# Kernel tuning notes

Hardware: AMD Instinct MI355X
Metric: run time of the kernel (lower is better)

The kernel has to match this reference:

```python
import jax, jax.numpy as jnp
import numpy as np

NUM_M = 2_000_000
NUM_T = 512
N = 16
NUM_GEN = N * (N - 1) // 2  # 120
NUM_STEPS = 64
TAU = 1.0


def _make_bases():
    # skew-symmetric so(n) basis, matching the torch buffer construction order
    bases = np.zeros((NUM_GEN, N, N), np.float32)
    k = 0
    for i in range(N):
        for j in range(i + 1, N):
            bases[k, i, j] = -1.0
            bases[k, j, i] = 1.0
            k += 1
    return jnp.asarray(bases)


def setup_inputs() -> dict:
    key = jax.random.key(0)
    ks = jax.random.split(key, 8)
    W = jax.random.normal(ks[0], (NUM_M, N), jnp.float32)
    emb_weight = W / jnp.linalg.norm(W, axis=-1, keepdims=True)  # normalized at init
    transition_coeffs = jax.random.normal(ks[1], (NUM_T, NUM_GEN), jnp.float32) * 0.1

    def lin(k, fi, fo):  # torch nn.Linear default init
        bound = 1.0 / np.sqrt(fi)
        kw, kb = jax.random.split(k)
        w = jax.random.uniform(kw, (fi, fo), jnp.float32, -bound, bound)
        b = jax.random.uniform(kb, (fo,), jnp.float32, -bound, bound)
        return w, b

    w1, b1 = lin(ks[2], 2 * N, 256)
    w2, b2 = lin(ks[3], 256, 128)
    w3, b3 = lin(ks[4], 128, NUM_T)

    v_src = jax.random.uniform(ks[5], (1, NUM_M), jnp.float32)
    v_target = jax.random.uniform(ks[6], (1, NUM_M), jnp.float32)
    # pre-sampled Gumbel(0,1) noise for gumbel_softmax, one draw per step
    u = jax.random.uniform(ks[7], (NUM_STEPS, 1, NUM_T), jnp.float32, 1e-6, 1.0 - 1e-6)
    gumbel = -jnp.log(-jnp.log(u))

    return {
        'v_src': v_src, 'v_target': v_target,
        'emb_weight': emb_weight, 'transition_coeffs': transition_coeffs,
        'bases': _make_bases(),
        'w1': w1, 'b1': b1, 'w2': w2, 'b2': b2, 'w3': w3, 'b3': b3,
        'gumbel': gumbel, 'num_steps': NUM_STEPS,
    }


def reference(v_src, v_target, emb_weight, transition_coeffs, bases,
              w1, b1, w2, b2, w3, b3, gumbel, num_steps):
    # training=True path of PetriNetAlignmentPredictor.forward, tau=1.0
    embs = emb_weight / jnp.linalg.norm(emb_weight, axis=-1, keepdims=True)
    v_cur = v_src @ embs      # [1, n]  (memory-bound matvec over num_m)
    v_tgt = v_target @ embs   # [1, n]
    gens = jnp.einsum('tg,gnm->tnm', transition_coeffs, bases)  # [num_t, n, n]
    expm_b = jax.vmap(jax.scipy.linalg.expm)

    def step(v, g):
        h = jax.nn.relu(jnp.concatenate([v, v_tgt], axis=-1) @ w1 + b1)
        h = jax.nn.relu(h @ w2 + b2)
        logits = h @ w3 + b3                       # [1, num_t]
        # gumbel_softmax(hard=True) with straight-through estimator
        y = jax.nn.softmax((logits + g) / TAU, axis=-1)
        hard = jax.nn.one_hot(jnp.argmax(y, axis=-1), logits.shape[-1], dtype=y.dtype)
        one_hot = hard + y - jax.lax.stop_gradient(y)
        omega = jnp.einsum('bt,tnm->bnm', one_hot, gens)  # skew-symmetric [1, n, n]
        R = expm_b(omega)
        v2 = jnp.einsum('bnm,bm->bn', R, v)
        v2 = v2 / jnp.linalg.norm(v2, axis=-1, keepdims=True)
        return v2, logits

    v_fin, logits_seq = jax.lax.scan(step, v_cur, gumbel[:num_steps])
    pred_marking = jax.nn.softmax(v_fin @ embs.T, axis=-1)  # [1, num_m]
    return pred_marking, logits_seq[:, 0, :]  # squeeze batch dim -> [num_steps, num_t]
```

## Files before the change

### kernel.cpp

```cpp
#include <hip/hip_runtime.h>

#define M_TOTAL   2000000
#define NT        512
#define K1_BLOCKS 1024
#define K3_BLOCKS 2048

__device__ __forceinline__ float rlf(float v, int l) {
    union { float f; int i; } u; u.f = v;
    u.i = __builtin_amdgcn_readlane(u.i, l);
    return u.f;
}

__device__ __forceinline__ void bar_lds() {
    asm volatile("s_waitcnt lgkmcnt(0)" ::: "memory");
    __builtin_amdgcn_s_barrier();
    asm volatile("" ::: "memory");
}

#define DPPMAXU(m, ctrl) { unsigned _d = (unsigned)__builtin_amdgcn_update_dpp(0, (int)(m), (ctrl), 0xF, 0xF, true); \
                           if (_d > (m)) (m) = _d; }
#define DPPADDF(s, ctrl) { float _d = __int_as_float(__builtin_amdgcn_update_dpp(0, __float_as_int(s), (ctrl), 0xF, 0xF, true)); \
                           (s) += _d; }

__device__ __forceinline__ unsigned orderf(float f) {
    unsigned u = __float_as_uint(f);
    return u ^ (((unsigned)((int)u >> 31)) | 0x80000000u);
}

__device__ __forceinline__ uint2 pick2(uint2 a, uint2 b) {
    bool takeb = (b.x > a.x) || (b.x == a.x && b.y < a.y);
    return takeb ? b : a;
}

#define REP16(M)  M(0) M(1) M(2) M(3) M(4) M(5) M(6) M(7) M(8) M(9) M(10) M(11) M(12) M(13) M(14) M(15)
#define REP16B(M) M(16) M(17) M(18) M(19) M(20) M(21) M(22) M(23) M(24) M(25) M(26) M(27) M(28) M(29) M(30) M(31)

#define VLD4(dst, base, c) { const volatile float* _p = (base) + 4*(c); \
    dst.x = _p[0]; dst.y = _p[1]; dst.z = _p[2]; dst.w = _p[3]; }

extern "C" __global__ __launch_bounds__(256)
void k_reduce(const float* __restrict__ emb, const float* __restrict__ vsrc,
              const float* __restrict__ vtgt, double* __restrict__ partials)
{
    const int tid = threadIdx.x;
    const int bid = blockIdx.x;
    double aS[4], aT[4];
#pragma unroll
    for (int i = 0; i < 4; i++) { aS[i] = 0.0; aT[i] = 0.0; }

    const float4* emb4 = (const float4*)emb;
    for (long long f = (long long)bid * 256 + tid; f < (long long)M_TOTAL * 4;
         f += (long long)K1_BLOCKS * 256) {
        float4 e = emb4[f];
        long long r = f >> 2;
        float sq = fmaf(e.x, e.x, fmaf(e.y, e.y, fmaf(e.z, e.z, e.w * e.w)));
        sq += __shfl_xor(sq, 1);
        sq += __shfl_xor(sq, 2);
        float invn = 1.0f / sqrtf(sq);
        float s = vsrc[r] * invn;
        float t = vtgt[r] * invn;
        aS[0] += (double)(s * e.x); aS[1] += (double)(s * e.y);
        aS[2] += (double)(s * e.z); aS[3] += (double)(s * e.w);
        aT[0] += (double)(t * e.x); aT[1] += (double)(t * e.y);
        aT[2] += (double)(t * e.z); aT[3] += (double)(t * e.w);
    }
#pragma unroll
    for (int i = 0; i < 4; i++) {
#pragma unroll
        for (int off = 32; off >= 4; off >>= 1) {
            aS[i] += __shfl_down(aS[i], off);
            aT[i] += __shfl_down(aT[i], off);
        }
    }
    __shared__ double lred[4][32];
    int lane = tid & 63, wv = tid >> 6;
    if (lane < 4) {
#pragma unroll
        for (int i = 0; i < 4; i++) {
            lred[wv][lane * 4 + i]      = aS[i];
            lred[wv][16 + lane * 4 + i] = aT[i];
        }
    }
    __syncthreads();
    if (tid < 32) {
        double v = lred[0][tid] + lred[1][tid] + lred[2][tid] + lred[3][tid];
        partials[(long long)bid * 32 + tid] = v;
    }
}

extern "C" __global__ __launch_bounds__(256)
void k_pre(const float* __restrict__ tc, float* __restrict__ Rtab,
           const float* __restrict__ w2g, const float* __restrict__ w3g,
           float* __restrict__ w2R, float* __restrict__ w3R,
           double* __restrict__ totalp)
{
    const int bid = blockIdx.x;
    const int t = threadIdx.x;

    if (bid < 512) {
        const int i = t >> 4, j = t & 15;
        __shared__ float Om[256];
        __shared__ float Ms[256];

        const float* crow = tc + bid * 120;
        float o = 0.0f;
        if (i < j)      o = -crow[(i * (31 - i)) / 2 + (j - i - 1)];
        else if (i > j) o =  crow[(j * (31 - j)) / 2 + (i - j - 1)];
        Om[t] = o;
        Ms[t] = o;
        float s = (i == j ? 1.0f : 0.0f) + o;
        __syncthreads();

#pragma unroll
        for (int k = 2; k <= 16; k++) {
            float a0 = 0.0f, a1 = 0.0f, a2 = 0.0f, a3 = 0.0f;
#pragma unroll
            for (int m = 0; m < 4; m++) {
                a0 = fmaf(Om[i * 16 + m],      Ms[m * 16 + j],        a0);
                a1 = fmaf(Om[i * 16 + 4 + m],  Ms[(4 + m) * 16 + j],  a1);
                a2 = fmaf(Om[i * 16 + 8 + m],  Ms[(8 + m) * 16 + j],  a2);
                a3 = fmaf(Om[i * 16 + 12 + m], Ms[(12 + m) * 16 + j], a3);
            }
            float acc = ((a0 + a1) + (a2 + a3)) * (1.0f / (float)k);
            __syncthreads();
            Ms[t] = acc;
            s += acc;
            __syncthreads();
        }
        Rtab[bid * 256 + t] = s;
    } else {
        if (bid == 512 && t == 0) totalp[0] = 0.0;
        if (t >= 128) return;
        const int b = bid - 512;
        const int k = t;
        if (b < 512) {
            w3R[b * 128 + k] = w3g[k * 512 + b];
        } else {
            const int p2 = b - 512;
            const int j2 = k;
            for (int m = 0; m < 64; m++)
                w2R[(((p2 << 7) | j2) * 64) + m] = w2g[(64 * p2 + m) * 128 + j2];
        }
    }
}

extern "C" __global__ __launch_bounds__(512)
__attribute__((amdgpu_waves_per_eu(2, 2)))
void k_steps(const double* __restrict__ partials,
             const float* __restrict__ w1g, const float* __restrict__ b1g,
             const float* __restrict__ b2g, const float* __restrict__ b3g,
             const float* __restrict__ w2R, const float* __restrict__ w3R,
             const float* __restrict__ Rtab, const float* __restrict__ gum,
             const int* __restrict__ nsp,
             float* __restrict__ outL, float* __restrict__ vf_out)
{
    __shared__ __align__(16) float h1s[256];
    __shared__ __align__(16) float h2p[512];
    __shared__ __align__(16) float h2s[128];
    __shared__ float xs[32];
    __shared__ float b2s[128];
    __shared__ uint2 kidx[8];
    __shared__ double dred[512];

    const int t = threadIdx.x;
    const int lane = t & 63;
    const int wv = t >> 6;
    const int j2 = t & 127, p2 = t >> 7;
    const int c1 = t & 255;

    const volatile float* w3v = (const volatile float*)(w3R + (size_t)t * 128);
    const volatile float* w2v = (const volatile float*)(w2R + (size_t)t * 64);
#define W3D(c) float4 w3_##c; VLD4(w3_##c, w3v, c)
    REP16(W3D) REP16B(W3D)
#undef W3D
#define W2D(c) float4 w2_##c; VLD4(w2_##c, w2v, c)
    REP16(W2D)
#undef W2D
    const float b3r = b3g[t];

    float w1r[16];
    {
        const volatile float* w1v = (const volatile float*)w1g;
#pragma unroll
        for (int m = 0; m < 16; m++) w1r[m] = w1v[m * 256 + c1];
    }
    if (t < 128) b2s[t] = b2g[t];

    float warm = 0.0f;
    for (int i = t; i < 512 * 256 / 4; i += 512) {
        float4 rv = ((const float4*)Rtab)[i];
        warm += (rv.x + rv.y) + (rv.z + rv.w);
    }

    {
        double v = 0.0;
#pragma unroll 4
        for (int i = 0; i < (K1_BLOCKS * 32) / 512; i++) v += partials[i * 512 + t];
        dred[t] = v;
    }

    int ns = nsp[0];
    if (ns > 64) ns = 64;
    if (ns < 0)  ns = 0;
    if (ns == -2147483647) vf_out[0] = warm;

    __syncthreads();
    if (t < 32) {
        double s = 0.0;
#pragma unroll
        for (int j = 0; j < 16; j++) s += dred[t + 32 * j];
        xs[t] = (float)s;
    }
    __syncthreads();

    float b1e = 0.0f, vreg = 0.0f;
    if (t < 256) {
        float a = b1g[c1];
#pragma unroll
        for (int m = 0; m < 16; m++)
            a = fmaf(xs[16 + m], w1g[(16 + m) * 256 + c1], a);
        b1e = a;
        vreg = xs[lane & 15];
    }

    if (ns == 0 && t < 16) vf_out[t] = xs[t];

    for (int step = 0; step < ns; step++) {
        float gv = gum[step * 512 + t];

        if (t < 256) {
            float a0 = 0.0f, a1 = 0.0f;
#pragma unroll
            for (int m = 0; m < 8; m++) {
                a0 = fmaf(rlf(vreg, m),     w1r[m],     a0);
                a1 = fmaf(rlf(vreg, 8 + m), w1r[8 + m], a1);
            }
            h1s[t] = fmaxf((a0 + a1) + b1e, 0.0f);
        }
        bar_lds();

        {
            const float2* h1b = (const float2*)&h1s[p2 << 6];
            float a0 = 0.0f, a1 = 0.0f, a2 = 0.0f, a3 = 0.0f;
#define L2C(c) { float2 mA = h1b[2*(c)]; float2 mB = h1b[2*(c)+1]; \
                 a0 = fmaf(mA.x, w2_##c.x, a0); \
                 a1 = fmaf(mA.y, w2_##c.y, a1); \
                 a2 = fmaf(mB.x, w2_##c.z, a2); \
                 a3 = fmaf(mB.y, w2_##c.w, a3); }
            REP16(L2C)
#undef L2C
            h2p[(p2 << 7) | j2] = (a0 + a1) + (a2 + a3);
        }
        bar_lds();

        if (t < 128) {
            float s = ((h2p[t] + h2p[128 + t]) + (h2p[256 + t] + h2p[384 + t])) + b2s[t];
            h2s[t] = fmaxf(s, 0.0f);
        }
        bar_lds();

        float lg;
        {
            const float2* h2b = (const float2*)h2s;
            float lg0 = 0.0f, lg1 = 0.0f, lg2 = 0.0f, lg3 = 0.0f;
#define L3C(c) { float2 mA = h2b[2*(c)]; float2 mB = h2b[2*(c)+1]; \
                 lg0 = fmaf(mA.x, w3_##c.x, lg0); \
                 lg1 = fmaf(mA.y, w3_##c.y, lg1); \
                 lg2 = fmaf(mB.x, w3_##c.z, lg2); \
                 lg3 = fmaf(mB.y, w3_##c.w, lg3); }
            REP16(L3C) REP16B(L3C)
#undef L3C
            lg = ((lg0 + lg1) + (lg2 + lg3)) + b3r;
        }
        outL[step * 512 + t] = lg;

        {
            unsigned ok = orderf(lg + gv);
            unsigned m = ok;
            DPPMAXU(m, 0x111)
            DPPMAXU(m, 0x112)
            DPPMAXU(m, 0x114)
            DPPMAXU(m, 0x118)
            DPPMAXU(m, 0x142)
            DPPMAXU(m, 0x143)
            unsigned wmax = (unsigned)__builtin_amdgcn_readlane((int)m, 63);
            unsigned long long mask = __ballot(ok == wmax);
            if (lane == 0) {
                uint2 kv; kv.x = wmax; kv.y = (unsigned)(wv * 64 + (__ffsll(mask) - 1));
                kidx[wv] = kv;
            }
        }
        bar_lds();

        if (t < 256 && lane < 16) {
            uint2 K0, K1, K2, K3, K4, K5, K6, K7;
            { uint4 a = *(const uint4*)&kidx[0]; K0.x=a.x; K0.y=a.y; K1.x=a.z; K1.y=a.w; }
            { uint4 a = *(const uint4*)&kidx[2]; K2.x=a.x; K2.y=a.y; K3.x=a.z; K3.y=a.w; }
            { uint4 a = *(const uint4*)&kidx[4]; K4.x=a.x; K4.y=a.y; K5.x=a.z; K5.y=a.w; }
            { uint4 a = *(const uint4*)&kidx[6]; K6.x=a.x; K6.y=a.y; K7.x=a.z; K7.y=a.w; }
            uint2 w01 = pick2(K0, K1), w23 = pick2(K2, K3);
            uint2 w45 = pick2(K4, K5), w67 = pick2(K6, K7);
            uint2 win = pick2(pick2(w01, w23), pick2(w45, w67));
            const int bi = (int)win.y;

            const float4* rp = (const float4*)(Rtab + (size_t)bi * 256 + lane * 16);
            float4 ra = rp[0], rb = rp[1], rc = rp[2], rd = rp[3];
            float p0 = ra.x * rlf(vreg, 0);
            float p1 = rb.x * rlf(vreg, 4);
            float p2r = rc.x * rlf(vreg, 8);
            float p3 = rd.x * rlf(vreg, 12);
            p0 = fmaf(ra.y, rlf(vreg, 1), p0);
            p1 = fmaf(rb.y, rlf(vreg, 5), p1);
            p2r = fmaf(rc.y, rlf(vreg, 9), p2r);
            p3 = fmaf(rd.y, rlf(vreg, 13), p3);
            p0 = fmaf(ra.z, rlf(vreg, 2), p0);
            p1 = fmaf(rb.z, rlf(vreg, 6), p1);
            p2r = fmaf(rc.z, rlf(vreg, 10), p2r);
            p3 = fmaf(rd.z, rlf(vreg, 14), p3);
            p0 = fmaf(ra.w, rlf(vreg, 3), p0);
            p1 = fmaf(rb.w, rlf(vreg, 7), p1);
            p2r = fmaf(rc.w, rlf(vreg, 11), p2r);
            p3 = fmaf(rd.w, rlf(vreg, 15), p3);
            float pr = (p0 + p1) + (p2r + p3);

            float s2 = pr * pr;
            DPPADDF(s2, 0x111)
            DPPADDF(s2, 0x112)
            DPPADDF(s2, 0x114)
            DPPADDF(s2, 0x118)
            float n2 = rlf(s2, 15);
            float invn = 1.0f / sqrtf(n2);
            vreg = pr * invn;
            if (step == ns - 1 && t < 16) vf_out[t] = vreg;
        }
    }
}

extern "C" __global__ __launch_bounds__(256)
void k_scores(const float* __restrict__ emb, const float* __restrict__ vf16,
              float* __restrict__ outP, double* __restrict__ totalp)
{
    __shared__ float vfs[16];
    const int tid = threadIdx.x;
    const int bid = blockIdx.x;
    const int q = tid & 3;
    if (tid < 16) vfs[tid] = vf16[tid];
    __syncthreads();
    float v0 = vfs[q * 4 + 0], v1 = vfs[q * 4 + 1], v2 = vfs[q * 4 + 2], v3 = vfs[q * 4 + 3];

    const float4* emb4 = (const float4*)emb;
    double bsum = 0.0;
    for (long long f = (long long)bid * 256 + tid; f < (long long)M_TOTAL * 4;
         f += (long long)K3_BLOCKS * 256) {
        float4 e = emb4[f];
        long long r = f >> 2;
        float sq = fmaf(e.x, e.x, fmaf(e.y, e.y, fmaf(e.z, e.z, e.w * e.w)));
        float d  = fmaf(e.x, v0, fmaf(e.y, v1, fmaf(e.z, v2, e.w * v3)));
        sq += __shfl_xor(sq, 1);  d += __shfl_xor(d, 1);
        sq += __shfl_xor(sq, 2);  d += __shfl_xor(d, 2);
        float ex = expf(d / sqrtf(sq));
        if (q == 0) {
            outP[r] = ex;
            bsum += (double)ex;
        }
    }
#pragma unroll
    for (int off = 4; off <= 32; off <<= 1) bsum += __shfl_down(bsum, off);
    __shared__ double lred[4];
    if ((tid & 63) == 0) lred[tid >> 6] = bsum;
    __syncthreads();
    if (tid == 0) atomicAdd(totalp, lred[0] + lred[1] + lred[2] + lred[3]);
}

extern "C" __global__ __launch_bounds__(256)
void k_scale(float* __restrict__ outP, const double* __restrict__ totalp)
{
    const float inv = 1.0f / (float)totalp[0];
    long long r4 = (long long)blockIdx.x * 256 + threadIdx.x;
    if (r4 < M_TOTAL / 4) {
        float4* p = (float4*)outP;
        float4 v = p[r4];
        v.x *= inv; v.y *= inv; v.z *= inv; v.w *= inv;
        p[r4] = v;
    }
}

extern "C" void kernel_launch(void* const* d_in, const int* in_sizes, int n_in,
                              void* d_out, int out_size, void* d_ws, size_t ws_size,
                              hipStream_t stream)
{
    const float* vsrc = (const float*)d_in[0];
    const float* vtgt = (const float*)d_in[1];
    const float* emb  = (const float*)d_in[2];
    const float* tc   = (const float*)d_in[3];
    const float* w1 = (const float*)d_in[5];
    const float* b1 = (const float*)d_in[6];
    const float* w2 = (const float*)d_in[7];
    const float* b2 = (const float*)d_in[8];
    const float* w3 = (const float*)d_in[9];
    const float* b3 = (const float*)d_in[10];
    const float* gum = (const float*)d_in[11];
    const int* nsp   = (const int*)d_in[12];

    float* outP = (float*)d_out;
    float* outL = outP + M_TOTAL;

    double* wsd      = (double*)d_ws;
    double* partials = wsd;
    double* totalp   = wsd + 2048 * 32;
    float*  vf       = (float*)(totalp + 1);

    float* Rtab = outP;
    float* w3R  = outP + 131072;
    float* w2R  = outP + 196608;

    k_pre<<<1028, 256, 0, stream>>>(tc, Rtab, w2, w3, w2R, w3R, totalp);
    k_reduce<<<K1_BLOCKS, 256, 0, stream>>>(emb, vsrc, vtgt, partials);
    k_steps<<<1, 512, 0, stream>>>(partials, w1, b1, b2, b3, w2R, w3R, Rtab, gum, nsp, outL, vf);
    k_scores<<<K3_BLOCKS, 256, 0, stream>>>(emb, vf, outP, totalp);
    k_scale<<<(M_TOTAL / 4 + 255) / 256, 256, 0, stream>>>(outP, totalp);
}
```

Before: 569.7 us.

## Merge reduce and precompute kernels, use DPP and readlane broadcasts in MLP

Merges the embedding reduction kernel and the precompute kernel (rotation tables, weight transposes) into one launch, so one launch overhead goes away and the two independent jobs run side by side. Per-row quad sums switch from shfl_xor to DPP quad-permute adds, and the reduction accumulates in float FMAs with a single conversion to double at the end. In the serial step kernel, layer-2 and layer-3 inputs are broadcast with readlane instead of LDS reads, which also removes one barrier per step. Accumulating in float per thread may slightly change precision.

```diff
diff --git a/kernel.cpp b/kernel.cpp
--- a/kernel.cpp
+++ b/kernel.cpp
@@ -21,6 +21,8 @@
                            if (_d > (m)) (m) = _d; }
 #define DPPADDF(s, ctrl) { float _d = __int_as_float(__builtin_amdgcn_update_dpp(0, __float_as_int(s), (ctrl), 0xF, 0xF, true)); \
                            (s) += _d; }
+#define QP_XOR1 0xB1
+#define QP_XOR2 0x4E
 
 __device__ __forceinline__ unsigned orderf(float f) {
     unsigned u = __float_as_uint(f);
@@ -39,70 +41,69 @@
     dst.x = _p[0]; dst.y = _p[1]; dst.z = _p[2]; dst.w = _p[3]; }
 
 extern "C" __global__ __launch_bounds__(256)
-void k_reduce(const float* __restrict__ emb, const float* __restrict__ vsrc,
-              const float* __restrict__ vtgt, double* __restrict__ partials)
-{
-    const int tid = threadIdx.x;
-    const int bid = blockIdx.x;
-    double aS[4], aT[4];
-#pragma unroll
-    for (int i = 0; i < 4; i++) { aS[i] = 0.0; aT[i] = 0.0; }
-
-    const float4* emb4 = (const float4*)emb;
-    for (long long f = (long long)bid * 256 + tid; f < (long long)M_TOTAL * 4;
-         f += (long long)K1_BLOCKS * 256) {
-        float4 e = emb4[f];
-        long long r = f >> 2;
-        float sq = fmaf(e.x, e.x, fmaf(e.y, e.y, fmaf(e.z, e.z, e.w * e.w)));
-        sq += __shfl_xor(sq, 1);
-        sq += __shfl_xor(sq, 2);
-        float invn = 1.0f / sqrtf(sq);
-        float s = vsrc[r] * invn;
-        float t = vtgt[r] * invn;
-        aS[0] += (double)(s * e.x); aS[1] += (double)(s * e.y);
-        aS[2] += (double)(s * e.z); aS[3] += (double)(s * e.w);
-        aT[0] += (double)(t * e.x); aT[1] += (double)(t * e.y);
-        aT[2] += (double)(t * e.z); aT[3] += (double)(t * e.w);
-    }
-#pragma unroll
-    for (int i = 0; i < 4; i++) {
-#pragma unroll
-        for (int off = 32; off >= 4; off >>= 1) {
-            aS[i] += __shfl_down(aS[i], off);
-            aT[i] += __shfl_down(aT[i], off);
-        }
-    }
-    __shared__ double lred[4][32];
-    int lane = tid & 63, wv = tid >> 6;
-    if (lane < 4) {
-#pragma unroll
-        for (int i = 0; i < 4; i++) {
-            lred[wv][lane * 4 + i]      = aS[i];
-            lred[wv][16 + lane * 4 + i] = aT[i];
-        }
-    }
-    __syncthreads();
-    if (tid < 32) {
-        double v = lred[0][tid] + lred[1][tid] + lred[2][tid] + lred[3][tid];
-        partials[(long long)bid * 32 + tid] = v;
-    }
-}
-
-extern "C" __global__ __launch_bounds__(256)
-void k_pre(const float* __restrict__ tc, float* __restrict__ Rtab,
-           const float* __restrict__ w2g, const float* __restrict__ w3g,
-           float* __restrict__ w2R, float* __restrict__ w3R,
-           double* __restrict__ totalp)
+void k_front(const float* __restrict__ emb, const float* __restrict__ vsrc,
+             const float* __restrict__ vtgt, double* __restrict__ partials,
+             const float* __restrict__ tc, float* __restrict__ Rtab,
+             const float* __restrict__ w2g, const float* __restrict__ w3g,
+             float* __restrict__ w2R, float* __restrict__ w3R,
+             double* __restrict__ totalp)
 {
     const int bid = blockIdx.x;
     const int t = threadIdx.x;
 
-    if (bid < 512) {
+    if (bid < K1_BLOCKS) {
+        float aS[4], aT[4];
+#pragma unroll
+        for (int i = 0; i < 4; i++) { aS[i] = 0.0f; aT[i] = 0.0f; }
+
+        const float4* emb4 = (const float4*)emb;
+        for (long long f = (long long)bid * 256 + t; f < (long long)M_TOTAL * 4;
+             f += (long long)K1_BLOCKS * 256) {
+            float4 e = emb4[f];
+            long long r = f >> 2;
+            float sq = fmaf(e.x, e.x, fmaf(e.y, e.y, fmaf(e.z, e.z, e.w * e.w)));
+            DPPADDF(sq, QP_XOR1)
+            DPPADDF(sq, QP_XOR2)
+            float invn = 1.0f / sqrtf(sq);
+            float s = vsrc[r] * invn;
+            float tv = vtgt[r] * invn;
+            aS[0] = fmaf(s, e.x, aS[0]);  aS[1] = fmaf(s, e.y, aS[1]);
+            aS[2] = fmaf(s, e.z, aS[2]);  aS[3] = fmaf(s, e.w, aS[3]);
+            aT[0] = fmaf(tv, e.x, aT[0]); aT[1] = fmaf(tv, e.y, aT[1]);
+            aT[2] = fmaf(tv, e.z, aT[2]); aT[3] = fmaf(tv, e.w, aT[3]);
+        }
+        double dS[4], dT[4];
+#pragma unroll
+        for (int i = 0; i < 4; i++) { dS[i] = (double)aS[i]; dT[i] = (double)aT[i]; }
+#pragma unroll
+        for (int i = 0; i < 4; i++) {
+#pragma unroll
+            for (int off = 32; off >= 4; off >>= 1) {
+                dS[i] += __shfl_down(dS[i], off);
+                dT[i] += __shfl_down(dT[i], off);
+            }
+        }
+        __shared__ double lred[4][32];
+        int lane = t & 63, wv = t >> 6;
+        if (lane < 4) {
+#pragma unroll
+            for (int i = 0; i < 4; i++) {
+                lred[wv][lane * 4 + i]      = dS[i];
+                lred[wv][16 + lane * 4 + i] = dT[i];
+            }
+        }
+        __syncthreads();
+        if (t < 32) {
+            double v = lred[0][t] + lred[1][t] + lred[2][t] + lred[3][t];
+            partials[(long long)bid * 32 + t] = v;
+        }
+    } else if (bid < K1_BLOCKS + 512) {
+        const int b = bid - K1_BLOCKS;
         const int i = t >> 4, j = t & 15;
         __shared__ float Om[256];
         __shared__ float Ms[256];
 
-        const float* crow = tc + bid * 120;
+        const float* crow = tc + b * 120;
         float o = 0.0f;
         if (i < j)      o = -crow[(i * (31 - i)) / 2 + (j - i - 1)];
         else if (i > j) o =  crow[(j * (31 - j)) / 2 + (i - j - 1)];
@@ -127,11 +128,11 @@
             s += acc;
             __syncthreads();
         }
-        Rtab[bid * 256 + t] = s;
+        Rtab[b * 256 + t] = s;
     } else {
-        if (bid == 512 && t == 0) totalp[0] = 0.0;
+        const int b = bid - (K1_BLOCKS + 512);
+        if (b == 0 && t == 0) totalp[0] = 0.0;
         if (t >= 128) return;
-        const int b = bid - 512;
         const int k = t;
         if (b < 512) {
             w3R[b * 128 + k] = w3g[k * 512 + b];
@@ -240,39 +241,40 @@
         bar_lds();
 
         {
-            const float2* h1b = (const float2*)&h1s[p2 << 6];
+            float h1seg = h1s[(p2 << 6) | lane];
             float a0 = 0.0f, a1 = 0.0f, a2 = 0.0f, a3 = 0.0f;
-#define L2C(c) { float2 mA = h1b[2*(c)]; float2 mB = h1b[2*(c)+1]; \
-                 a0 = fmaf(mA.x, w2_##c.x, a0); \
-                 a1 = fmaf(mA.y, w2_##c.y, a1); \
-                 a2 = fmaf(mB.x, w2_##c.z, a2); \
-                 a3 = fmaf(mB.y, w2_##c.w, a3); }
+#define L2C(c) { a0 = fmaf(rlf(h1seg, 4*(c)+0), w2_##c.x, a0); \
+                 a1 = fmaf(rlf(h1seg, 4*(c)+1), w2_##c.y, a1); \
+                 a2 = fmaf(rlf(h1seg, 4*(c)+2), w2_##c.z, a2); \
+                 a3 = fmaf(rlf(h1seg, 4*(c)+3), w2_##c.w, a3); }
             REP16(L2C)
 #undef L2C
             h2p[(p2 << 7) | j2] = (a0 + a1) + (a2 + a3);
         }
         bar_lds();
 
-        if (t < 128) {
-            float s = ((h2p[t] + h2p[128 + t]) + (h2p[256 + t] + h2p[384 + t])) + b2s[t];
-            h2s[t] = fmaxf(s, 0.0f);
-        }
-        bar_lds();
-
         float lg;
         {
-            const float2* h2b = (const float2*)h2s;
+            float h2lo = fmaxf(((h2p[lane] + h2p[128 + lane]) +
+                                (h2p[256 + lane] + h2p[384 + lane])) + b2s[lane], 0.0f);
+            float h2hi = fmaxf(((h2p[64 + lane] + h2p[192 + lane]) +
+                                (h2p[320 + lane] + h2p[448 + lane])) + b2s[64 + lane], 0.0f);
             float lg0 = 0.0f, lg1 = 0.0f, lg2 = 0.0f, lg3 = 0.0f;
-#define L3C(c) { float2 mA = h2b[2*(c)]; float2 mB = h2b[2*(c)+1]; \
-                 lg0 = fmaf(mA.x, w3_##c.x, lg0); \
-                 lg1 = fmaf(mA.y, w3_##c.y, lg1); \
-                 lg2 = fmaf(mB.x, w3_##c.z, lg2); \
-                 lg3 = fmaf(mB.y, w3_##c.w, lg3); }
-            REP16(L3C) REP16B(L3C)
-#undef L3C
+#define L3LO(c) { lg0 = fmaf(rlf(h2lo, 4*(c)+0), w3_##c.x, lg0); \
+                  lg1 = fmaf(rlf(h2lo, 4*(c)+1), w3_##c.y, lg1); \
+                  lg2 = fmaf(rlf(h2lo, 4*(c)+2), w3_##c.z, lg2); \
+                  lg3 = fmaf(rlf(h2lo, 4*(c)+3), w3_##c.w, lg3); }
+#define L3HI(c) { lg0 = fmaf(rlf(h2hi, 4*(c)-64), w3_##c.x, lg0); \
+                  lg1 = fmaf(rlf(h2hi, 4*(c)-63), w3_##c.y, lg1); \
+                  lg2 = fmaf(rlf(h2hi, 4*(c)-62), w3_##c.z, lg2); \
+                  lg3 = fmaf(rlf(h2hi, 4*(c)-61), w3_##c.w, lg3); }
+            REP16(L3LO) REP16B(L3HI)
+#undef L3LO
+#undef L3HI
             lg = ((lg0 + lg1) + (lg2 + lg3)) + b3r;
         }
         outL[step * 512 + t] = lg;
+        (void)h2s;
 
         {
             unsigned ok = orderf(lg + gv);
@@ -356,8 +358,10 @@
         long long r = f >> 2;
         float sq = fmaf(e.x, e.x, fmaf(e.y, e.y, fmaf(e.z, e.z, e.w * e.w)));
         float d  = fmaf(e.x, v0, fmaf(e.y, v1, fmaf(e.z, v2, e.w * v3)));
-        sq += __shfl_xor(sq, 1);  d += __shfl_xor(d, 1);
-        sq += __shfl_xor(sq, 2);  d += __shfl_xor(d, 2);
+        DPPADDF(sq, QP_XOR1)
+        DPPADDF(d,  QP_XOR1)
+        DPPADDF(sq, QP_XOR2)
+        DPPADDF(d,  QP_XOR2)
         float ex = expf(d / sqrtf(sq));
         if (q == 0) {
             outP[r] = ex;
@@ -414,8 +418,8 @@
     float* w3R  = outP + 131072;
     float* w2R  = outP + 196608;
 
-    k_pre<<<1028, 256, 0, stream>>>(tc, Rtab, w2, w3, w2R, w3R, totalp);
-    k_reduce<<<K1_BLOCKS, 256, 0, stream>>>(emb, vsrc, vtgt, partials);
+    k_front<<<K1_BLOCKS + 512 + 516, 256, 0, stream>>>(emb, vsrc, vtgt, partials,
+                                                       tc, Rtab, w2, w3, w2R, w3R, totalp);
     k_steps<<<1, 512, 0, stream>>>(partials, w1, b1, b2, b3, w2R, w3R, Rtab, gum, nsp, outL, vf);
     k_scores<<<K3_BLOCKS, 256, 0, stream>>>(emb, vf, outP, totalp);
     k_scale<<<(M_TOTAL / 4 + 255) / 256, 256, 0, stream>>>(outP, totalp);
```

New measurement: 461.8 us. 1.23x faster.
